# Kernel tuning notes

Hardware: AMD Instinct MI355X
Metric: run time of the kernel (lower is better)

The kernel has to match this reference:

```python
import jax, jax.numpy as jnp
import numpy as np

N = 100000   # nodes
E = 1600000  # edges (avg degree 16)
D = 64       # embedding_dim
H = 64       # hidden_dim


def setup_inputs() -> dict:
    key = jax.random.key(0)
    k = jax.random.split(key, 4)
    embedding = jax.random.normal(k[0], (N, D), dtype=jnp.float32)
    edge_index = jax.random.randint(k[1], (2, E), 0, N, dtype=jnp.int64)
    W1 = jax.random.normal(k[2], (D, H), dtype=jnp.float32) / np.sqrt(D).astype(np.float32)
    b1 = jnp.zeros((H,), jnp.float32)
    W2 = jax.random.normal(k[3], (H, D), dtype=jnp.float32) / np.sqrt(H).astype(np.float32)
    b2 = jnp.zeros((D,), jnp.float32)
    return {"embedding": embedding, "edge_index": edge_index,
            "W1": W1, "b1": b1, "W2": W2, "b2": b2}


def _gcn_layer(x, src, dst, norm, W, b, n):
    # linear transform first (small GEMM), then normalized scatter-add aggregation
    h = x @ W                                   # [n, out]
    msg = h[src] * norm[:, None]                # gather + scale, [E+n, out]
    out = jax.ops.segment_sum(msg, dst, num_segments=n)
    return out + b


def reference(embedding, edge_index, W1, b1, W2, b2):
    n = embedding.shape[0]
    loop = jnp.arange(n)
    # GCNConv adds self-loops before normalization
    src = jnp.concatenate([edge_index[0], loop])
    dst = jnp.concatenate([edge_index[1], loop])
    deg = jax.ops.segment_sum(jnp.ones_like(dst, dtype=embedding.dtype), dst, num_segments=n)
    dinv = jax.lax.rsqrt(deg)                   # deg >= 1 thanks to self-loops
    norm = dinv[src] * dinv[dst]                # symmetric D^-1/2 A_hat D^-1/2
    h1 = jax.nn.relu(_gcn_layer(embedding, src, dst, norm, W1, b1, n))
    h2 = jax.nn.relu(_gcn_layer(h1, src, dst, norm, W2, b2, n))
    return h2
```

## Files before the change

kernel.cpp:

```cpp
#include <hip/hip_runtime.h>


#define NBMAX 512
#define BCAP  5120
#define CHUNK 4096

__global__ void zero_int_kernel(int* __restrict__ p, int m) {
    int i = blockIdx.x * blockDim.x + threadIdx.x;
    if (i < m) p[i] = 0;
}

__global__ __launch_bounds__(256) void bucket_scatter_kernel(
        const int* __restrict__ src, const int* __restrict__ dst,
        int* __restrict__ bucket_fill, unsigned int* __restrict__ bucketed,
        int E, int nb) {
    __shared__ int cnt[NBMAX];
    __shared__ int sc[NBMAX];
    __shared__ int exc[NBMAX + 1];
    __shared__ int rk[NBMAX];
    __shared__ int gb[NBMAX];
    __shared__ unsigned int pk[CHUNK];
    __shared__ unsigned short bid[CHUNK];
    int t = threadIdx.x;
    int base = blockIdx.x * CHUNK;
    for (int i = t; i < NBMAX; i += 256) { cnt[i] = 0; rk[i] = 0; }
    __syncthreads();
    unsigned int s[16]; int b[16];
#pragma unroll
    for (int j = 0; j < 16; ++j) {
        int e = base + j * 256 + t;
        if (e < E) {
            int d = dst[e];
            b[j] = d >> 8;
            s[j] = (unsigned int)src[e] | ((unsigned int)(d & 255) << 17);
            atomicAdd(&cnt[b[j]], 1);
        } else b[j] = -1;
    }
    __syncthreads();
    sc[t] = cnt[t];
    sc[t + 256] = cnt[t + 256];
    __syncthreads();
    for (int off = 1; off < NBMAX; off <<= 1) {
        int v0 = (t >= off) ? sc[t - off] : 0;
        int v1 = sc[t + 256 - off];
        __syncthreads();
        sc[t] += v0; sc[t + 256] += v1;
        __syncthreads();
    }
    if (t == 0) exc[0] = 0;
    exc[t + 1] = sc[t];
    exc[t + 257] = sc[t + 256];
    __syncthreads();
#pragma unroll
    for (int j = 0; j < 16; ++j) {
        if (b[j] >= 0) {
            int r = atomicAdd(&rk[b[j]], 1);
            int pos = exc[b[j]] + r;
            pk[pos] = s[j];
            bid[pos] = (unsigned short)b[j];
        }
    }
    for (int i = t; i < nb; i += 256)
        if (cnt[i] > 0) gb[i] = atomicAdd(&bucket_fill[i], cnt[i]);
    __syncthreads();
    int m = exc[nb];
    for (int idx = t; idx < m; idx += 256) {
        int bb = bid[idx];
        int off = gb[bb] + (idx - exc[bb]);
        if (off < BCAP) bucketed[(size_t)bb * BCAP + off] = pk[idx];
    }
}

__global__ void bucket_scan_kernel(const int* __restrict__ bucket_fill,
                                   int* __restrict__ bucket_base,
                                   int* __restrict__ row_ptr, int nb, int n) {
    __shared__ int sm[NBMAX];
    int t = threadIdx.x;
    int v = (t < nb) ? bucket_fill[t] : 0;
    sm[t] = v; __syncthreads();
    for (int off = 1; off < NBMAX; off <<= 1) {
        int x = (t >= off) ? sm[t - off] : 0;
        __syncthreads();
        sm[t] += x;
        __syncthreads();
    }
    if (t < nb) bucket_base[t] = sm[t] - v;
    if (t == nb - 1) { bucket_base[nb] = sm[t]; row_ptr[n] = sm[t]; }
}

__global__ __launch_bounds__(256) void csr_build_kernel(
        const unsigned int* __restrict__ bucketed, const int* __restrict__ bucket_fill,
        const int* __restrict__ bucket_base, int* __restrict__ row_ptr,
        float* __restrict__ dinv, int* __restrict__ col_src, int n) {
    __shared__ int cnt[256], rk2[256], sc2[256], lofs[256];
    __shared__ unsigned int ent[BCAP];
    __shared__ int cout[BCAP];
    int b = blockIdx.x, t = threadIdx.x;
    int m = bucket_fill[b]; if (m > BCAP) m = BCAP;
    int gbase = bucket_base[b];
    cnt[t] = 0; rk2[t] = 0;
    __syncthreads();
    const unsigned int* ebase = bucketed + (size_t)b * BCAP;
    for (int i = t; i < m; i += 256) {
        unsigned int p = ebase[i];
        ent[i] = p;
        atomicAdd(&cnt[p >> 17], 1);
    }
    __syncthreads();
    int v = cnt[t];
    sc2[t] = v; __syncthreads();
    for (int off = 1; off < 256; off <<= 1) {
        int x = (t >= off) ? sc2[t - off] : 0;
        __syncthreads();
        sc2[t] += x;
        __syncthreads();
    }
    lofs[t] = sc2[t] - v;
    __syncthreads();
    int node = (b << 8) + t;
    if (node < n) {
        row_ptr[node] = gbase + lofs[t];
        dinv[node] = rsqrtf((float)(v + 1));
    }
    for (int i = t; i < m; i += 256) {
        unsigned int p = ent[i];
        int dl = p >> 17;
        int r = atomicAdd(&rk2[dl], 1);
        cout[lofs[dl] + r] = (int)(p & 0x1FFFF);
    }
    __syncthreads();
    for (int i = t; i < m; i += 256) col_src[gbase + i] = cout[i];
}

__global__ __launch_bounds__(256, 4) void gemm_scale_kernel(
        const float* __restrict__ x, const float* __restrict__ W,
        const float* __restrict__ dinv, float* __restrict__ g, int n) {
    __shared__ float4 ws4[64 * 16];
    int t = threadIdx.x;
    const float4* W4 = (const float4*)W;
#pragma unroll
    for (int j = 0; j < 4; ++j) ws4[j * 256 + t] = W4[j * 256 + t];
    __syncthreads();
    int cg = t & 7;
    int rg = t >> 3;
    int row0 = blockIdx.x * 128;
    const float4* x4 = (const float4*)x;
    int r[4];
#pragma unroll
    for (int j = 0; j < 4; ++j) {
        int rr = row0 + rg + 32 * j;
        r[j] = (rr < n) ? rr : 0;
    }
    float4 acc[4][2];
#pragma unroll
    for (int j = 0; j < 4; ++j) {
        acc[j][0] = make_float4(0.f, 0.f, 0.f, 0.f);
        acc[j][1] = make_float4(0.f, 0.f, 0.f, 0.f);
    }
#pragma unroll 2
    for (int kq = 0; kq < 16; ++kq) {
        float4 xv[4];
#pragma unroll
        for (int j = 0; j < 4; ++j) xv[j] = x4[(size_t)r[j] * 16 + kq];
#pragma unroll
        for (int kk = 0; kk < 4; ++kk) {
            int k = kq * 4 + kk;
            float4 w0 = ws4[k * 16 + 2 * cg];
            float4 w1 = ws4[k * 16 + 2 * cg + 1];
#pragma unroll
            for (int j = 0; j < 4; ++j) {
                float xk = ((const float*)&xv[j])[kk];
                acc[j][0].x = fmaf(xk, w0.x, acc[j][0].x);
                acc[j][0].y = fmaf(xk, w0.y, acc[j][0].y);
                acc[j][0].z = fmaf(xk, w0.z, acc[j][0].z);
                acc[j][0].w = fmaf(xk, w0.w, acc[j][0].w);
                acc[j][1].x = fmaf(xk, w1.x, acc[j][1].x);
                acc[j][1].y = fmaf(xk, w1.y, acc[j][1].y);
                acc[j][1].z = fmaf(xk, w1.z, acc[j][1].z);
                acc[j][1].w = fmaf(xk, w1.w, acc[j][1].w);
            }
        }
    }
    float4* g4 = (float4*)g;
#pragma unroll
    for (int j = 0; j < 4; ++j) {
        int rr = row0 + rg + 32 * j;
        if (rr < n) {
            float d = dinv[rr];
            float4 o0, o1;
            o0.x = acc[j][0].x * d; o0.y = acc[j][0].y * d;
            o0.z = acc[j][0].z * d; o0.w = acc[j][0].w * d;
            o1.x = acc[j][1].x * d; o1.y = acc[j][1].y * d;
            o1.z = acc[j][1].z * d; o1.w = acc[j][1].w * d;
            g4[(size_t)rr * 16 + 2 * cg]     = o0;
            g4[(size_t)rr * 16 + 2 * cg + 1] = o1;
        }
    }
}

__global__ __launch_bounds__(256) void aggregate_kernel(
        const float* __restrict__ g, const int* __restrict__ row_ptr,
        const int* __restrict__ col_src, const float* __restrict__ dinv,
        const float* __restrict__ bias, float* __restrict__ out, int n) {
    int wid = (blockIdx.x * 256 + threadIdx.x) >> 6;
    int lane = threadIdx.x & 63;
    int grp = lane >> 4;
    int l16 = lane & 15;
    if (wid >= n) return;
    const float4* g4 = (const float4*)g;
    float4 acc = make_float4(0.f, 0.f, 0.f, 0.f);
    int beg = row_ptr[wid];
    int end = row_ptr[wid + 1];
    int i = beg + grp;
    for (; i + 12 < end; i += 16) {
        int s0 = col_src[i];
        int s1 = col_src[i + 4];
        int s2 = col_src[i + 8];
        int s3 = col_src[i + 12];
        float4 v0 = g4[(size_t)s0 * 16 + l16];
        float4 v1 = g4[(size_t)s1 * 16 + l16];
        float4 v2 = g4[(size_t)s2 * 16 + l16];
        float4 v3 = g4[(size_t)s3 * 16 + l16];
        acc.x += (v0.x + v1.x) + (v2.x + v3.x);
        acc.y += (v0.y + v1.y) + (v2.y + v3.y);
        acc.z += (v0.z + v1.z) + (v2.z + v3.z);
        acc.w += (v0.w + v1.w) + (v2.w + v3.w);
    }
    for (; i < end; i += 4) {
        int s = col_src[i];
        float4 v = g4[(size_t)s * 16 + l16];
        acc.x += v.x; acc.y += v.y; acc.z += v.z; acc.w += v.w;
    }
    acc.x += __shfl_xor(acc.x, 16, 64);
    acc.y += __shfl_xor(acc.y, 16, 64);
    acc.z += __shfl_xor(acc.z, 16, 64);
    acc.w += __shfl_xor(acc.w, 16, 64);
    acc.x += __shfl_xor(acc.x, 32, 64);
    acc.y += __shfl_xor(acc.y, 32, 64);
    acc.z += __shfl_xor(acc.z, 32, 64);
    acc.w += __shfl_xor(acc.w, 32, 64);
    if (grp == 0) {
        float4 self = g4[(size_t)wid * 16 + l16];
        acc.x += self.x; acc.y += self.y; acc.z += self.z; acc.w += self.w;
        float d = dinv[wid];
        float4 b = ((const float4*)bias)[l16];
        float4 r;
        r.x = fmaxf(fmaf(acc.x, d, b.x), 0.f);
        r.y = fmaxf(fmaf(acc.y, d, b.y), 0.f);
        r.z = fmaxf(fmaf(acc.z, d, b.z), 0.f);
        r.w = fmaxf(fmaf(acc.w, d, b.w), 0.f);
        ((float4*)out)[(size_t)wid * 16 + l16] = r;
    }
}

extern "C" void kernel_launch(void* const* d_in, const int* in_sizes, int n_in,
                              void* d_out, int out_size, void* d_ws, size_t ws_size,
                              hipStream_t stream) {
    const float* embedding = (const float*)d_in[0];
    const int*   edge_idx  = (const int*)d_in[1];
    const float* W1        = (const float*)d_in[2];
    const float* b1        = (const float*)d_in[3];
    const float* W2        = (const float*)d_in[4];
    const float* b2        = (const float*)d_in[5];
    float* out = (float*)d_out;

    const int n = in_sizes[0] / 64;
    const int E = in_sizes[1] / 2;
    const int* src = edge_idx;
    const int* dst = edge_idx + E;
    const int nb = (n + 255) >> 8;

    char* w = (char*)d_ws;
    auto alloc = [&](size_t bytes) {
        char* p = w;
        w += (bytes + 255) & ~(size_t)255;
        return p;
    };
    int*   row_ptr     = (int*)  alloc(((size_t)n + 1) * 4);
    float* dinv        = (float*)alloc((size_t)n * 4);
    int*   col_src     = (int*)  alloc((size_t)E * 4);
    int*   bucket_fill = (int*)  alloc((size_t)nb * 4);
    int*   bucket_base = (int*)  alloc(((size_t)nb + 1) * 4);
    char*  gshare      = alloc((size_t)n * 64 * 4);
    float* g           = (float*)gshare;
    unsigned int* bucketed = (unsigned int*)gshare;

    zero_int_kernel<<<(nb + 255) / 256, 256, 0, stream>>>(bucket_fill, nb);
    bucket_scatter_kernel<<<(E + CHUNK - 1) / CHUNK, 256, 0, stream>>>(
        src, dst, bucket_fill, bucketed, E, nb);
    bucket_scan_kernel<<<1, NBMAX, 0, stream>>>(bucket_fill, bucket_base, row_ptr, nb, n);
    csr_build_kernel<<<nb, 256, 0, stream>>>(
        bucketed, bucket_fill, bucket_base, row_ptr, dinv, col_src, n);

    const int gemm_blocks = (n + 127) / 128;
    const int agg_blocks  = (int)(((size_t)n * 64 + 255) / 256);

    gemm_scale_kernel<<<gemm_blocks, 256, 0, stream>>>(embedding, W1, dinv, g, n);
    aggregate_kernel<<<agg_blocks, 256, 0, stream>>>(g, row_ptr, col_src, dinv, b1, out, n);
    gemm_scale_kernel<<<gemm_blocks, 256, 0, stream>>>(out, W2, dinv, g, n);
    aggregate_kernel<<<agg_blocks, 256, 0, stream>>>(g, row_ptr, col_src, dinv, b2, out, n);
}
```

Measured before the change: 282.9 us.

## Store transformed features in fp16 and widen bucket scatter blocks to 512 threads

The GEMM now writes the scaled per-node features as half precision, and the aggregation gathers 8 halves per lane with 8 neighbor groups per wavefront, accumulating in fp32. This halves the bytes moved by the gather-heavy aggregation, which is the memory-bound core. Separately, the bucket scatter kernel moves to 512-thread blocks with 8192-edge chunks, which simplifies the scan to one element per thread. Half-precision storage adds rounding error to the intermediate messages.

```diff
diff --git a/kernel.cpp b/kernel.cpp
--- a/kernel.cpp
+++ b/kernel.cpp
@@ -1,16 +1,17 @@
 #include <hip/hip_runtime.h>
+#include <hip/hip_fp16.h>
 
 
 #define NBMAX 512
 #define BCAP  5120
-#define CHUNK 4096
+#define CHUNK 8192
 
 __global__ void zero_int_kernel(int* __restrict__ p, int m) {
     int i = blockIdx.x * blockDim.x + threadIdx.x;
     if (i < m) p[i] = 0;
 }
 
-__global__ __launch_bounds__(256) void bucket_scatter_kernel(
+__global__ __launch_bounds__(512) void bucket_scatter_kernel(
         const int* __restrict__ src, const int* __restrict__ dst,
         int* __restrict__ bucket_fill, unsigned int* __restrict__ bucketed,
         int E, int nb) {
@@ -23,12 +24,12 @@
     __shared__ unsigned short bid[CHUNK];
     int t = threadIdx.x;
     int base = blockIdx.x * CHUNK;
-    for (int i = t; i < NBMAX; i += 256) { cnt[i] = 0; rk[i] = 0; }
+    cnt[t] = 0; rk[t] = 0;
     __syncthreads();
     unsigned int s[16]; int b[16];
 #pragma unroll
     for (int j = 0; j < 16; ++j) {
-        int e = base + j * 256 + t;
+        int e = base + j * 512 + t;
         if (e < E) {
             int d = dst[e];
             b[j] = d >> 8;
@@ -38,18 +39,15 @@
     }
     __syncthreads();
     sc[t] = cnt[t];
-    sc[t + 256] = cnt[t + 256];
     __syncthreads();
     for (int off = 1; off < NBMAX; off <<= 1) {
-        int v0 = (t >= off) ? sc[t - off] : 0;
-        int v1 = sc[t + 256 - off];
-        __syncthreads();
-        sc[t] += v0; sc[t + 256] += v1;
+        int x = (t >= off) ? sc[t - off] : 0;
+        __syncthreads();
+        sc[t] += x;
         __syncthreads();
     }
     if (t == 0) exc[0] = 0;
     exc[t + 1] = sc[t];
-    exc[t + 257] = sc[t + 256];
     __syncthreads();
 #pragma unroll
     for (int j = 0; j < 16; ++j) {
@@ -60,11 +58,10 @@
             bid[pos] = (unsigned short)b[j];
         }
     }
-    for (int i = t; i < nb; i += 256)
-        if (cnt[i] > 0) gb[i] = atomicAdd(&bucket_fill[i], cnt[i]);
-    __syncthreads();
-    int m = exc[nb];
-    for (int idx = t; idx < m; idx += 256) {
+    if (t < nb && cnt[t] > 0) gb[t] = atomicAdd(&bucket_fill[t], cnt[t]);
+    __syncthreads();
+    int m = exc[NBMAX];
+    for (int idx = t; idx < m; idx += 512) {
         int bb = bid[idx];
         int off = gb[bb] + (idx - exc[bb]);
         if (off < BCAP) bucketed[(size_t)bb * BCAP + off] = pk[idx];
@@ -134,7 +131,7 @@
 
 __global__ __launch_bounds__(256, 4) void gemm_scale_kernel(
         const float* __restrict__ x, const float* __restrict__ W,
-        const float* __restrict__ dinv, float* __restrict__ g, int n) {
+        const float* __restrict__ dinv, __half* __restrict__ g, int n) {
     __shared__ float4 ws4[64 * 16];
     int t = threadIdx.x;
     const float4* W4 = (const float4*)W;
@@ -181,75 +178,87 @@
             }
         }
     }
-    float4* g4 = (float4*)g;
+    uint4* g16 = (uint4*)g;
 #pragma unroll
     for (int j = 0; j < 4; ++j) {
         int rr = row0 + rg + 32 * j;
         if (rr < n) {
             float d = dinv[rr];
-            float4 o0, o1;
-            o0.x = acc[j][0].x * d; o0.y = acc[j][0].y * d;
-            o0.z = acc[j][0].z * d; o0.w = acc[j][0].w * d;
-            o1.x = acc[j][1].x * d; o1.y = acc[j][1].y * d;
-            o1.z = acc[j][1].z * d; o1.w = acc[j][1].w * d;
-            g4[(size_t)rr * 16 + 2 * cg]     = o0;
-            g4[(size_t)rr * 16 + 2 * cg + 1] = o1;
+            __half2 h0 = __floats2half2_rn(acc[j][0].x * d, acc[j][0].y * d);
+            __half2 h1 = __floats2half2_rn(acc[j][0].z * d, acc[j][0].w * d);
+            __half2 h2 = __floats2half2_rn(acc[j][1].x * d, acc[j][1].y * d);
+            __half2 h3 = __floats2half2_rn(acc[j][1].z * d, acc[j][1].w * d);
+            uint4 u;
+            u.x = *(unsigned int*)&h0;
+            u.y = *(unsigned int*)&h1;
+            u.z = *(unsigned int*)&h2;
+            u.w = *(unsigned int*)&h3;
+            g16[(size_t)rr * 8 + cg] = u;
         }
     }
 }
 
+__device__ __forceinline__ void acc_add_h8(float* acc, uint4 u) {
+    const __half2* hp = (const __half2*)&u;
+#pragma unroll
+    for (int q = 0; q < 4; ++q) {
+        float2 f = __half22float2(hp[q]);
+        acc[2 * q]     += f.x;
+        acc[2 * q + 1] += f.y;
+    }
+}
+
 __global__ __launch_bounds__(256) void aggregate_kernel(
-        const float* __restrict__ g, const int* __restrict__ row_ptr,
+        const __half* __restrict__ g, const int* __restrict__ row_ptr,
         const int* __restrict__ col_src, const float* __restrict__ dinv,
         const float* __restrict__ bias, float* __restrict__ out, int n) {
     int wid = (blockIdx.x * 256 + threadIdx.x) >> 6;
     int lane = threadIdx.x & 63;
-    int grp = lane >> 4;
-    int l16 = lane & 15;
+    int grp = lane >> 3;
+    int l8  = lane & 7;
     if (wid >= n) return;
-    const float4* g4 = (const float4*)g;
-    float4 acc = make_float4(0.f, 0.f, 0.f, 0.f);
+    const uint4* g16 = (const uint4*)g;
+    float acc[8] = {0.f, 0.f, 0.f, 0.f, 0.f, 0.f, 0.f, 0.f};
     int beg = row_ptr[wid];
     int end = row_ptr[wid + 1];
     int i = beg + grp;
-    for (; i + 12 < end; i += 16) {
+    for (; i + 8 < end; i += 16) {
         int s0 = col_src[i];
-        int s1 = col_src[i + 4];
-        int s2 = col_src[i + 8];
-        int s3 = col_src[i + 12];
-        float4 v0 = g4[(size_t)s0 * 16 + l16];
-        float4 v1 = g4[(size_t)s1 * 16 + l16];
-        float4 v2 = g4[(size_t)s2 * 16 + l16];
-        float4 v3 = g4[(size_t)s3 * 16 + l16];
-        acc.x += (v0.x + v1.x) + (v2.x + v3.x);
-        acc.y += (v0.y + v1.y) + (v2.y + v3.y);
-        acc.z += (v0.z + v1.z) + (v2.z + v3.z);
-        acc.w += (v0.w + v1.w) + (v2.w + v3.w);
-    }
-    for (; i < end; i += 4) {
+        int s1 = col_src[i + 8];
+        uint4 u0 = g16[(size_t)s0 * 8 + l8];
+        uint4 u1 = g16[(size_t)s1 * 8 + l8];
+        acc_add_h8(acc, u0);
+        acc_add_h8(acc, u1);
+    }
+    for (; i < end; i += 8) {
         int s = col_src[i];
-        float4 v = g4[(size_t)s * 16 + l16];
-        acc.x += v.x; acc.y += v.y; acc.z += v.z; acc.w += v.w;
-    }
-    acc.x += __shfl_xor(acc.x, 16, 64);
-    acc.y += __shfl_xor(acc.y, 16, 64);
-    acc.z += __shfl_xor(acc.z, 16, 64);
-    acc.w += __shfl_xor(acc.w, 16, 64);
-    acc.x += __shfl_xor(acc.x, 32, 64);
-    acc.y += __shfl_xor(acc.y, 32, 64);
-    acc.z += __shfl_xor(acc.z, 32, 64);
-    acc.w += __shfl_xor(acc.w, 32, 64);
+        uint4 u = g16[(size_t)s * 8 + l8];
+        acc_add_h8(acc, u);
+    }
+#pragma unroll
+    for (int c = 0; c < 8; ++c) {
+        acc[c] += __shfl_xor(acc[c], 8, 64);
+        acc[c] += __shfl_xor(acc[c], 16, 64);
+        acc[c] += __shfl_xor(acc[c], 32, 64);
+    }
     if (grp == 0) {
-        float4 self = g4[(size_t)wid * 16 + l16];
-        acc.x += self.x; acc.y += self.y; acc.z += self.z; acc.w += self.w;
+        uint4 us = g16[(size_t)wid * 8 + l8];
+        acc_add_h8(acc, us);
         float d = dinv[wid];
-        float4 b = ((const float4*)bias)[l16];
-        float4 r;
-        r.x = fmaxf(fmaf(acc.x, d, b.x), 0.f);
-        r.y = fmaxf(fmaf(acc.y, d, b.y), 0.f);
-        r.z = fmaxf(fmaf(acc.z, d, b.z), 0.f);
-        r.w = fmaxf(fmaf(acc.w, d, b.w), 0.f);
-        ((float4*)out)[(size_t)wid * 16 + l16] = r;
+        const float4* b4 = (const float4*)bias;
+        float4 ba = b4[2 * l8], bb = b4[2 * l8 + 1];
+        float4 o0, o1;
+        o0.x = fmaxf(fmaf(acc[0], d, ba.x), 0.f);
+        o0.y = fmaxf(fmaf(acc[1], d, ba.y), 0.f);
+        o0.z = fmaxf(fmaf(acc[2], d, ba.z), 0.f);
+        o0.w = fmaxf(fmaf(acc[3], d, ba.w), 0.f);
+        o1.x = fmaxf(fmaf(acc[4], d, bb.x), 0.f);
+        o1.y = fmaxf(fmaf(acc[5], d, bb.y), 0.f);
+        o1.z = fmaxf(fmaf(acc[6], d, bb.z), 0.f);
+        o1.w = fmaxf(fmaf(acc[7], d, bb.w), 0.f);
+        float4* o4 = (float4*)out;
+        o4[(size_t)wid * 16 + 2 * l8]     = o0;
+        o4[(size_t)wid * 16 + 2 * l8 + 1] = o1;
     }
 }
 
@@ -282,11 +291,11 @@
     int*   bucket_fill = (int*)  alloc((size_t)nb * 4);
     int*   bucket_base = (int*)  alloc(((size_t)nb + 1) * 4);
     char*  gshare      = alloc((size_t)n * 64 * 4);
-    float* g           = (float*)gshare;
+    __half* g          = (__half*)gshare;
     unsigned int* bucketed = (unsigned int*)gshare;
 
     zero_int_kernel<<<(nb + 255) / 256, 256, 0, stream>>>(bucket_fill, nb);
-    bucket_scatter_kernel<<<(E + CHUNK - 1) / CHUNK, 256, 0, stream>>>(
+    bucket_scatter_kernel<<<(E + CHUNK - 1) / CHUNK, 512, 0, stream>>>(
         src, dst, bucket_fill, bucketed, E, nb);
     bucket_scan_kernel<<<1, NBMAX, 0, stream>>>(bucket_fill, bucket_base, row_ptr, nb, n);
     csr_build_kernel<<<nb, 256, 0, stream>>>(
```

New measurement: 240.6 us. 15.0% less time.
